# Kernel tuning notes

Measured on AMD Instinct MI355X. Metric: run time of the kernel, lower is better.

Reference implementation:

```python
import jax, jax.numpy as jnp
import numpy as np
import math

HEADS = 4
DK = 64            # dim // heads
TEMP = 1.0
LMAX = 2048        # max segment length (for padded ragged attention)


def setup_inputs() -> dict:
    key = jax.random.key(0)
    ks = jax.random.split(key, 6)
    T, H, B = 1024, 256, 16
    # ragged lengths alternating 2048/1024 -> N = 24576
    lengths = np.tile(np.array([2048, 1024], dtype=np.int64), B // 2)
    N = int(lengths.sum())
    s = 1.0 / math.sqrt(H)
    return {
        "go_mat": jax.random.normal(ks[0], (T, H), jnp.float32),
        "node_h": jax.random.normal(ks[1], (N, H), jnp.float32),
        "Wq": jax.random.normal(ks[2], (H, H), jnp.float32) * s,
        "Wk": jax.random.normal(ks[3], (H, H), jnp.float32) * s,
        "Wv": jax.random.normal(ks[4], (H, H), jnp.float32) * s,
        "Wproj": jax.random.normal(ks[5], (H, H), jnp.float32) * s,
        "num_nodes_per_graph": jnp.asarray(lengths),
    }


def reference(go_mat, node_h, Wq, Wk, Wv, Wproj, num_nodes_per_graph):
    lengths = num_nodes_per_graph
    B = lengths.shape[0]
    N, H = node_h.shape
    T = go_mat.shape[0]

    # segment bookkeeping: graph id and within-graph offset for each node
    cum = jnp.cumsum(lengths)                       # [B]
    starts = cum - lengths                          # [B]
    g = jnp.searchsorted(cum, jnp.arange(N), side="right")  # [N] graph id
    off = jnp.arange(N) - starts[g]                 # [N] position within graph

    # projections (torch Linear: x @ W.T)
    Q = (go_mat @ Wq.T).reshape(T, HEADS, DK).transpose(1, 0, 2)   # [h,T,dk]
    K = node_h @ Wk.T                                              # [N,H]
    V = node_h @ Wv.T

    # scatter packed nodes into padded [B, Lmax, H]
    Kp = jnp.zeros((B, LMAX, H), K.dtype).at[g, off].set(K)
    Vp = jnp.zeros((B, LMAX, H), V.dtype).at[g, off].set(V)
    Kp = Kp.reshape(B, LMAX, HEADS, DK).transpose(0, 2, 1, 3)      # [B,h,L,dk]
    Vp = Vp.reshape(B, LMAX, HEADS, DK).transpose(0, 2, 1, 3)

    scores = jnp.einsum("htd,bhld->bhtl", Q, Kp) / (math.sqrt(DK) * TEMP)
    valid = jnp.arange(LMAX)[None, :] < lengths[:, None]           # [B,L]
    scores = jnp.where(valid[:, None, None, :], scores, jnp.float32(-1e30))
    attn = jax.nn.softmax(scores, axis=-1)                         # [B,h,T,L]

    ctx = jnp.einsum("bhtl,bhld->bhtd", attn, Vp)                  # [B,h,T,dk]
    ctx = ctx.transpose(0, 2, 1, 3).reshape(B, T, H)               # [B,T,H]
    return ctx @ Wproj.T
```

## Files before the change

### kernel.cpp

```cpp
#include <hip/hip_runtime.h>
#include <math.h>

#define HEADS 4
#define DK 64
#define HD 256

typedef __attribute__((ext_vector_type(8))) __bf16 bf16x8;
typedef __attribute__((ext_vector_type(4))) float floatx4;

__device__ __forceinline__ ushort f2bf(float f) {
  union { float f; unsigned u; } x; x.f = f;
  return (ushort)((x.u + 0x7FFF + ((x.u >> 16) & 1)) >> 16);
}

#if __has_builtin(__builtin_amdgcn_exp2f)
#define EXP2(x) __builtin_amdgcn_exp2f(x)
#else
#define EXP2(x) exp2f(x)
#endif

__device__ __forceinline__ unsigned pack_bf2(float lo, float hi) {
  union { float f; unsigned u; } a, b;
  a.f = lo; b.f = hi;
  return __builtin_amdgcn_perm(b.u + 0x8000u, a.u + 0x8000u, 0x07060302u);
}

#define GLDS(g, l) __builtin_amdgcn_global_load_lds(                      \
    (const __attribute__((address_space(1))) unsigned*)(g),               \
    (__attribute__((address_space(3))) unsigned*)(l), 16, 0, 0)

__global__ __launch_bounds__(256) void cvt_all(const float* __restrict__ go,
                                               const float* __restrict__ nh,
                                               ushort* __restrict__ gobf,
                                               ushort* __restrict__ nodebf,
                                               int T, int N) {
  const int idx = blockIdx.x * 256 + threadIdx.x;
  const int row = idx >> 5, gr = idx & 31;
  if (row >= T + N) return;
  const float* x; ushort* y; int r;
  if (row < T) { x = go; y = gobf; r = row; }
  else         { x = nh; y = nodebf; r = row - T; }
  const int chunk = gr >> 3, g = gr & 7;
  const float* src = x + (size_t)r * 256 + gr * 8;
  float4 a = *(const float4*)src;
  float4 bq = *(const float4*)(src + 4);
  const int phys = g ^ (r & 7);
  ushort* dst = y + (size_t)r * 256 + chunk * 64 + phys * 8;
  ushort4 o0 = {f2bf(a.x), f2bf(a.y), f2bf(a.z), f2bf(a.w)};
  ushort4 o1 = {f2bf(bq.x), f2bf(bq.y), f2bf(bq.z), f2bf(bq.w)};
  *(ushort4*)dst = o0;
  *(ushort4*)(dst + 4) = o1;
}

__global__ __launch_bounds__(256) void cvt_swz_w(const float* __restrict__ w0,
                                                 const float* __restrict__ w1,
                                                 const float* __restrict__ w2,
                                                 const float* __restrict__ w3,
                                                 ushort* __restrict__ y) {
  const float* srcs[4] = {w0, w1, w2, w3};
  const float* x = srcs[blockIdx.y];
  ushort* yo = y + (size_t)blockIdx.y * HD * HD;
  const int idx = blockIdx.x * 256 + threadIdx.x;
  const int row = idx >> 5, gr = idx & 31;
  const int chunk = gr >> 3, g = gr & 7;
  const float* src = x + (size_t)row * 256 + gr * 8;
  float4 a = *(const float4*)src;
  float4 bq = *(const float4*)(src + 4);
  const int phys = g ^ (row & 7);
  ushort* dst = yo + (size_t)row * 256 + chunk * 64 + phys * 8;
  ushort4 o0 = {f2bf(a.x), f2bf(a.y), f2bf(a.z), f2bf(a.w)};
  ushort4 o1 = {f2bf(bq.x), f2bf(bq.y), f2bf(bq.z), f2bf(bq.w)};
  *(ushort4*)dst = o0;
  *(ushort4*)(dst + 4) = o1;
}

template <int MODE>
__global__ __launch_bounds__(256) void gemm_bf16(const ushort* __restrict__ A,
                                                 const ushort* __restrict__ W,
                                                 ushort* __restrict__ C, int M,
                                                 int ldc) {
  __shared__ __align__(16) ushort As[128 * 64];
  __shared__ __align__(16) ushort Ws[64 * 64];
  const int tid = threadIdx.x, lane = tid & 63, w = tid >> 6;
  const int quad = lane >> 4, l15 = lane & 15;
  const int m0 = blockIdx.x * 128, n0 = blockIdx.y * 64;
  const int wm = w & 1, wn = w >> 1;

  floatx4 acc[4][2];
#pragma unroll
  for (int mt = 0; mt < 4; ++mt)
#pragma unroll
    for (int nt = 0; nt < 2; ++nt) acc[mt][nt] = (floatx4){0.f, 0.f, 0.f, 0.f};

  for (int k0 = 0; k0 < 256; k0 += 64) {
    __syncthreads();
#pragma unroll
    for (int t = 0; t < 4; ++t)
      GLDS(A + (size_t)(m0 + w * 32 + t * 8 + (lane >> 3)) * 256 + k0 + (lane & 7) * 8,
           &As[(w * 32 + t * 8) * 64]);
#pragma unroll
    for (int t = 0; t < 2; ++t)
      GLDS(W + (size_t)(n0 + w * 16 + t * 8 + (lane >> 3)) * 256 + k0 + (lane & 7) * 8,
           &Ws[(w * 16 + t * 8) * 64]);
    __syncthreads();

    bf16x8 af[4][2], bfr[2][2];
#pragma unroll
    for (int kk = 0; kk < 2; ++kk) {
      const int pg = ((kk * 4 + quad) ^ (l15 & 7)) * 8;
#pragma unroll
      for (int mt = 0; mt < 4; ++mt)
        af[mt][kk] = *(const bf16x8*)&As[(wm * 64 + mt * 16 + l15) * 64 + pg];
#pragma unroll
      for (int nt = 0; nt < 2; ++nt)
        bfr[nt][kk] = *(const bf16x8*)&Ws[(wn * 32 + nt * 16 + l15) * 64 + pg];
    }
#pragma unroll
    for (int kk = 0; kk < 2; ++kk)
#pragma unroll
      for (int mt = 0; mt < 4; ++mt)
#pragma unroll
        for (int nt = 0; nt < 2; ++nt)
          acc[mt][nt] = __builtin_amdgcn_mfma_f32_16x16x32_bf16(
              af[mt][kk], bfr[nt][kk], acc[mt][nt], 0, 0, 0);
  }

#pragma unroll
  for (int mt = 0; mt < 4; ++mt)
#pragma unroll
    for (int nt = 0; nt < 2; ++nt) {
      const int col = n0 + wn * 32 + nt * 16 + l15;
      if (MODE == 2) {
        const int d = col & 63;
        const int g = mt * 2 + (quad >> 1);
        const int node = m0 + wm * 64 + (g ^ (d & 7)) * 8 + (quad & 1) * 4;
        ushort4 o = {f2bf(acc[mt][nt][0]), f2bf(acc[mt][nt][1]),
                     f2bf(acc[mt][nt][2]), f2bf(acc[mt][nt][3])};
        *(ushort4*)&C[(size_t)col * ldc + node] = o;
      } else {
#pragma unroll
        for (int r = 0; r < 4; ++r) {
          const int row = m0 + wm * 64 + mt * 16 + quad * 4 + r;
          if (MODE == 3) {
            ((float*)C)[(size_t)row * 256 + col] = acc[mt][nt][r];
          } else {
            int cc = col;
            if (MODE == 1)
              cc = (col & ~63) | (((((col >> 3) & 7) ^ (row & 7))) << 3) | (col & 7);
            C[(size_t)row * 256 + cc] = f2bf(acc[mt][nt][r]);
          }
        }
      }
    }
}

__global__ __launch_bounds__(256, 3) void attn_split(
    const ushort* __restrict__ Qb, const ushort* __restrict__ Kg,
    const ushort* __restrict__ Vt, const int* __restrict__ lens,
    float* __restrict__ Opart, float* __restrict__ Lpart,
    int T, int N, int Bc) {
  __shared__ __align__(16) ushort Ks[2][64 * 64];
  __shared__ __align__(16) ushort Vs[2][64 * 64];
  __shared__ __align__(16) ushort Ps[4 * 32 * 72];

  const int tid = threadIdx.x, lane = tid & 63, wave = tid >> 6;
  const int quad = lane >> 4, l15 = lane & 15;
  const int h = blockIdx.y;

  int z = blockIdx.z, b, start = 0, len = 0, off = -1;
  for (b = 0; b < Bc; ++b) {
    len = lens[b];
    const int s = (len + 1023) >> 10;
    if (z < s) { off = z << 10; break; }
    z -= s; start += len;
  }
  if (off < 0) return;
  const int kcnt = min(1024, len - off);
  const int kbeg = start + off;

  const int q0 = blockIdx.x * 128 + wave * 32;
  bf16x8 qb[2][2];
#pragma unroll
  for (int qt = 0; qt < 2; ++qt)
#pragma unroll
    for (int kk = 0; kk < 2; ++kk)
      qb[qt][kk] = *(const bf16x8*)(Qb + (size_t)(q0 + qt * 16 + l15) * 256 +
                                    h * 64 + kk * 32 + quad * 8);

  floatx4 o[2][4];
#pragma unroll
  for (int qt = 0; qt < 2; ++qt)
#pragma unroll
    for (int nt = 0; nt < 4; ++nt) o[qt][nt] = (floatx4){0.f, 0.f, 0.f, 0.f};
  float lsum[2] = {0.f, 0.f};

  const float sc = 0.18033688011112042f;
  ushort* pw = &Ps[wave * 32 * 72];

  const int srow = lane >> 3;
  const int scol = (lane & 7) * 8;

  GLDS(Kg + (size_t)(kbeg + wave * 8 + srow) * 256 + h * 64 + scol,
       &Ks[0][(wave * 8) * 64]);
  GLDS(Kg + (size_t)(kbeg + wave * 8 + 32 + srow) * 256 + h * 64 + scol,
       &Ks[0][(wave * 8 + 32) * 64]);
  GLDS(Vt + (size_t)(h * 64 + wave * 8 + srow) * (size_t)N + kbeg + scol,
       &Vs[0][(wave * 8) * 64]);
  GLDS(Vt + (size_t)(h * 64 + wave * 8 + 32 + srow) * (size_t)N + kbeg + scol,
       &Vs[0][(wave * 8 + 32) * 64]);

  int buf = 0;
  for (int j0 = 0; j0 < kcnt; j0 += 64, buf ^= 1) {
    __syncthreads();
    const int jn = j0 + 64;
    if (jn < kcnt) {
      GLDS(Kg + (size_t)(kbeg + jn + wave * 8 + srow) * 256 + h * 64 + scol,
           &Ks[buf ^ 1][(wave * 8) * 64]);
      GLDS(Kg + (size_t)(kbeg + jn + wave * 8 + 32 + srow) * 256 + h * 64 + scol,
           &Ks[buf ^ 1][(wave * 8 + 32) * 64]);
      GLDS(Vt + (size_t)(h * 64 + wave * 8 + srow) * (size_t)N + kbeg + jn + scol,
           &Vs[buf ^ 1][(wave * 8) * 64]);
      GLDS(Vt + (size_t)(h * 64 + wave * 8 + 32 + srow) * (size_t)N + kbeg + jn + scol,
           &Vs[buf ^ 1][(wave * 8 + 32) * 64]);
    }

    floatx4 st[4][2];
#pragma unroll
    for (int t = 0; t < 4; ++t)
#pragma unroll
      for (int qt = 0; qt < 2; ++qt) st[t][qt] = (floatx4){0.f, 0.f, 0.f, 0.f};
#pragma unroll
    for (int kk = 0; kk < 2; ++kk) {
#pragma unroll
      for (int t = 0; t < 4; ++t) {
        bf16x8 kf = *(const bf16x8*)&Ks[buf][(t * 16 + l15) * 64 +
                                            ((kk * 4 + quad) ^ (l15 & 7)) * 8];
        st[t][0] = __builtin_amdgcn_mfma_f32_16x16x32_bf16(kf, qb[0][kk], st[t][0], 0, 0, 0);
        st[t][1] = __builtin_amdgcn_mfma_f32_16x16x32_bf16(kf, qb[1][kk], st[t][1], 0, 0, 0);
      }
    }

    if (jn <= kcnt) {
#pragma unroll
      for (int t = 0; t < 4; ++t)
#pragma unroll
        for (int qt = 0; qt < 2; ++qt) {
          float p[4];
#pragma unroll
          for (int r = 0; r < 4; ++r) p[r] = EXP2(fmaf(st[t][qt][r], sc, -32.0f));
          lsum[qt] += (p[0] + p[1]) + (p[2] + p[3]);
          uint2 pk = {pack_bf2(p[0], p[1]), pack_bf2(p[2], p[3])};
          *(uint2*)&pw[(qt * 16 + l15) * 72 + t * 16 + quad * 4] = pk;
        }
    } else {
#pragma unroll
      for (int t = 0; t < 4; ++t)
#pragma unroll
        for (int qt = 0; qt < 2; ++qt) {
          float p[4];
#pragma unroll
          for (int r = 0; r < 4; ++r) {
            const bool v = (j0 + t * 16 + quad * 4 + r) < kcnt;
            p[r] = v ? EXP2(fmaf(st[t][qt][r], sc, -32.0f)) : 0.0f;
          }
          lsum[qt] += (p[0] + p[1]) + (p[2] + p[3]);
          uint2 pk = {pack_bf2(p[0], p[1]), pack_bf2(p[2], p[3])};
          *(uint2*)&pw[(qt * 16 + l15) * 72 + t * 16 + quad * 4] = pk;
        }
    }

#pragma unroll
    for (int ks = 0; ks < 2; ++ks) {
      bf16x8 pa0 = *(const bf16x8*)&pw[l15 * 72 + ks * 32 + quad * 8];
      bf16x8 pa1 = *(const bf16x8*)&pw[(16 + l15) * 72 + ks * 32 + quad * 8];
#pragma unroll
      for (int nt = 0; nt < 4; ++nt) {
        bf16x8 vf = *(const bf16x8*)&Vs[buf][(nt * 16 + l15) * 64 +
                                            ((ks * 4 + quad) ^ (l15 & 7)) * 8];
        o[0][nt] = __builtin_amdgcn_mfma_f32_16x16x32_bf16(pa0, vf, o[0][nt], 0, 0, 0);
        o[1][nt] = __builtin_amdgcn_mfma_f32_16x16x32_bf16(pa1, vf, o[1][nt], 0, 0, 0);
      }
    }
  }

  const int part = (blockIdx.z * HEADS + h) * (T >> 7) + blockIdx.x;
  float* op = Opart + (size_t)part * (128 * 64);
#pragma unroll
  for (int qt = 0; qt < 2; ++qt) {
#pragma unroll
    for (int nt = 0; nt < 4; ++nt)
#pragma unroll
      for (int r = 0; r < 4; ++r)
        op[(wave * 32 + qt * 16 + quad * 4 + r) * 64 + nt * 16 + l15] = o[qt][nt][r];
    float lt = lsum[qt];
    lt += __shfl_xor(lt, 16);
    lt += __shfl_xor(lt, 32);
    if (lane < 16)
      Lpart[(size_t)part * 128 + wave * 32 + qt * 16 + lane] = lt;
  }
}

__global__ __launch_bounds__(256) void combine(const float* __restrict__ Opart,
                                               const float* __restrict__ Lpart,
                                               const int* __restrict__ lens,
                                               ushort* __restrict__ ctxb, int T) {
  const int t = threadIdx.x;
  const int row = blockIdx.x * 64 + (t >> 2);
  const int h = t & 3;
  const int b = row / T;
  const int tq = row - b * T;
  const int qx = tq >> 7, qr = tq & 127;
  const int QX = T >> 7;
  int z0 = 0;
  for (int i = 0; i < b; ++i) z0 += (lens[i] + 1023) >> 10;
  const int ns = (lens[b] + 1023) >> 10;

  float l = 0.f;
  float4 acc[16];
#pragma unroll
  for (int g = 0; g < 16; ++g) acc[g] = make_float4(0.f, 0.f, 0.f, 0.f);
  for (int s = 0; s < ns; ++s) {
    const size_t part = (size_t)((z0 + s) * HEADS + h) * QX + qx;
    l += Lpart[part * 128 + qr];
    const float4* src = (const float4*)(Opart + part * 8192 + (size_t)qr * 64);
#pragma unroll
    for (int g = 0; g < 16; ++g) {
      float4 v = src[g];
      acc[g].x += v.x; acc[g].y += v.y; acc[g].z += v.z; acc[g].w += v.w;
    }
  }
  const float inv = 1.0f / l;
  ushort* dst = ctxb + (size_t)row * 256 + h * 64;
#pragma unroll
  for (int gg = 0; gg < 8; ++gg) {
    const float4 a = acc[gg * 2], c = acc[gg * 2 + 1];
    const int phys = gg ^ (row & 7);
    ushort4 o0 = {f2bf(a.x * inv), f2bf(a.y * inv), f2bf(a.z * inv), f2bf(a.w * inv)};
    ushort4 o1 = {f2bf(c.x * inv), f2bf(c.y * inv), f2bf(c.z * inv), f2bf(c.w * inv)};
    *(ushort4*)&dst[phys * 8] = o0;
    *(ushort4*)&dst[phys * 8 + 4] = o1;
  }
}

extern "C" void kernel_launch(void* const* d_in, const int* in_sizes, int n_in,
                              void* d_out, int out_size, void* d_ws, size_t ws_size,
                              hipStream_t stream) {
  const float* go     = (const float*)d_in[0];
  const float* node_h = (const float*)d_in[1];
  const float* Wq     = (const float*)d_in[2];
  const float* Wk     = (const float*)d_in[3];
  const float* Wv     = (const float*)d_in[4];
  const float* Wproj  = (const float*)d_in[5];
  const int*   lens   = (const int*)d_in[6];

  const int T = in_sizes[0] / HD;
  const int N = in_sizes[1] / HD;
  const int B = in_sizes[6];
  const int NSPL = N >> 10;
  const int QX = T / 128;

  char* p = (char*)d_ws;
  ushort* Kgb  = (ushort*)p;  p += (size_t)N * HD * 2;
  ushort* Vtb  = (ushort*)p;  p += (size_t)N * HD * 2;
  ushort* Qbf  = (ushort*)p;  p += (size_t)T * HD * 2;
  ushort* gobf = (ushort*)p;  p += (size_t)T * HD * 2;
  ushort* ctxb = (ushort*)p;  p += (size_t)B * T * HD * 2;
  ushort* wbf  = (ushort*)p;  p += (size_t)4 * HD * HD * 2;
  ushort* wqbf = wbf;
  ushort* wkbf = wbf + (size_t)HD * HD;
  ushort* wvbf = wbf + (size_t)2 * HD * HD;
  ushort* wpbf = wbf + (size_t)3 * HD * HD;
  ushort* nodebf = (ushort*)p;
  float* Opart = (float*)p;   p += (size_t)NSPL * HEADS * QX * 8192 * 4;
  float* Lpart = (float*)p;   p += (size_t)NSPL * HEADS * QX * 128 * 4;

  cvt_all<<<((T + N) * 32 + 255) / 256, 256, 0, stream>>>(go, node_h, gobf, nodebf, T, N);
  cvt_swz_w<<<dim3(32, 4), 256, 0, stream>>>(Wq, Wk, Wv, Wproj, wbf);

  gemm_bf16<0><<<dim3(T / 128, 4), 256, 0, stream>>>(gobf, wqbf, Qbf, T, 0);
  gemm_bf16<1><<<dim3(N / 128, 4), 256, 0, stream>>>(nodebf, wkbf, Kgb, N, 0);
  gemm_bf16<2><<<dim3(N / 128, 4), 256, 0, stream>>>(nodebf, wvbf, Vtb, N, N);

  attn_split<<<dim3(QX, HEADS, NSPL), 256, 0, stream>>>(Qbf, Kgb, Vtb, lens,
                                                        Opart, Lpart, T, N, B);
  combine<<<(B * T) / 64, 256, 0, stream>>>(Opart, Lpart, lens, ctxb, T);

  gemm_bf16<3><<<dim3((B * T) / 128, 4), 256, 0, stream>>>(ctxb, wpbf, (ushort*)d_out, B * T, 0);
}
```

Measured before the change: 167.0 us.

## Fuse conversion and QKV launches, halve attention split size, store bf16 partials

Merges the input and weight conversion kernels into one launch and the three QKV projection GEMMs into a single launch. The attention key splits shrink from 1024 to 512 for more blocks, and K/V double buffering is dropped to raise occupancy (launch bound 5). The P tile in LDS becomes XOR-swizzled instead of padded. Partial outputs are stored as bf16 instead of fp32, and the combine kernel uses twice as many threads. This cuts launch overhead and partial-output traffic, but loses load/compute overlap in attention and adds bf16 rounding to the partials.

```diff
diff --git a/kernel.cpp b/kernel.cpp
--- a/kernel.cpp
+++ b/kernel.cpp
@@ -29,63 +29,42 @@
     (const __attribute__((address_space(1))) unsigned*)(g),               \
     (__attribute__((address_space(3))) unsigned*)(l), 16, 0, 0)
 
-__global__ __launch_bounds__(256) void cvt_all(const float* __restrict__ go,
-                                               const float* __restrict__ nh,
-                                               ushort* __restrict__ gobf,
-                                               ushort* __restrict__ nodebf,
-                                               int T, int N) {
+__global__ __launch_bounds__(256) void cvt_fused(
+    const float* __restrict__ go, const float* __restrict__ nh,
+    const float* __restrict__ w0, const float* __restrict__ w1,
+    const float* __restrict__ w2, const float* __restrict__ w3,
+    ushort* __restrict__ gobf, ushort* __restrict__ nodebf,
+    ushort* __restrict__ wbf, int T, int N) {
   const int idx = blockIdx.x * 256 + threadIdx.x;
   const int row = idx >> 5, gr = idx & 31;
-  if (row >= T + N) return;
-  const float* x; ushort* y; int r;
-  if (row < T) { x = go; y = gobf; r = row; }
-  else         { x = nh; y = nodebf; r = row - T; }
+  if (row >= T + N + 4 * 256) return;
+  const float* x; ushort* y; int r = row;
+  if (row < T) { x = go; y = gobf; }
+  else if (row < T + N) { x = nh; y = nodebf; r = row - T; }
+  else {
+    const int wr = row - T - N, wi = wr >> 8;
+    r = wr & 255;
+    x = (wi == 0) ? w0 : (wi == 1) ? w1 : (wi == 2) ? w2 : w3;
+    y = wbf + (size_t)wi * HD * HD;
+  }
   const int chunk = gr >> 3, g = gr & 7;
   const float* src = x + (size_t)r * 256 + gr * 8;
   float4 a = *(const float4*)src;
   float4 bq = *(const float4*)(src + 4);
-  const int phys = g ^ (r & 7);
-  ushort* dst = y + (size_t)r * 256 + chunk * 64 + phys * 8;
+  ushort* dst = y + (size_t)r * 256 + chunk * 64 + (g ^ (r & 7)) * 8;
   ushort4 o0 = {f2bf(a.x), f2bf(a.y), f2bf(a.z), f2bf(a.w)};
   ushort4 o1 = {f2bf(bq.x), f2bf(bq.y), f2bf(bq.z), f2bf(bq.w)};
   *(ushort4*)dst = o0;
   *(ushort4*)(dst + 4) = o1;
 }
 
-__global__ __launch_bounds__(256) void cvt_swz_w(const float* __restrict__ w0,
-                                                 const float* __restrict__ w1,
-                                                 const float* __restrict__ w2,
-                                                 const float* __restrict__ w3,
-                                                 ushort* __restrict__ y) {
-  const float* srcs[4] = {w0, w1, w2, w3};
-  const float* x = srcs[blockIdx.y];
-  ushort* yo = y + (size_t)blockIdx.y * HD * HD;
-  const int idx = blockIdx.x * 256 + threadIdx.x;
-  const int row = idx >> 5, gr = idx & 31;
-  const int chunk = gr >> 3, g = gr & 7;
-  const float* src = x + (size_t)row * 256 + gr * 8;
-  float4 a = *(const float4*)src;
-  float4 bq = *(const float4*)(src + 4);
-  const int phys = g ^ (row & 7);
-  ushort* dst = yo + (size_t)row * 256 + chunk * 64 + phys * 8;
-  ushort4 o0 = {f2bf(a.x), f2bf(a.y), f2bf(a.z), f2bf(a.w)};
-  ushort4 o1 = {f2bf(bq.x), f2bf(bq.y), f2bf(bq.z), f2bf(bq.w)};
-  *(ushort4*)dst = o0;
-  *(ushort4*)(dst + 4) = o1;
-}
-
-template <int MODE>
-__global__ __launch_bounds__(256) void gemm_bf16(const ushort* __restrict__ A,
-                                                 const ushort* __restrict__ W,
-                                                 ushort* __restrict__ C, int M,
-                                                 int ldc) {
-  __shared__ __align__(16) ushort As[128 * 64];
-  __shared__ __align__(16) ushort Ws[64 * 64];
-  const int tid = threadIdx.x, lane = tid & 63, w = tid >> 6;
-  const int quad = lane >> 4, l15 = lane & 15;
-  const int m0 = blockIdx.x * 128, n0 = blockIdx.y * 64;
+__device__ __forceinline__ void gemm_tile(const ushort* __restrict__ A,
+                                          const ushort* __restrict__ W,
+                                          ushort* __restrict__ C, int m0,
+                                          int n0, int mode, int ldc,
+                                          ushort* As, ushort* Ws, int lane,
+                                          int w, int quad, int l15) {
   const int wm = w & 1, wn = w >> 1;
-
   floatx4 acc[4][2];
 #pragma unroll
   for (int mt = 0; mt < 4; ++mt)
@@ -130,7 +109,7 @@
 #pragma unroll
     for (int nt = 0; nt < 2; ++nt) {
       const int col = n0 + wn * 32 + nt * 16 + l15;
-      if (MODE == 2) {
+      if (mode == 2) {
         const int d = col & 63;
         const int g = mt * 2 + (quad >> 1);
         const int node = m0 + wm * 64 + (g ^ (d & 7)) * 8 + (quad & 1) * 4;
@@ -141,11 +120,11 @@
 #pragma unroll
         for (int r = 0; r < 4; ++r) {
           const int row = m0 + wm * 64 + mt * 16 + quad * 4 + r;
-          if (MODE == 3) {
+          if (mode == 3) {
             ((float*)C)[(size_t)row * 256 + col] = acc[mt][nt][r];
           } else {
             int cc = col;
-            if (MODE == 1)
+            if (mode == 1)
               cc = (col & ~63) | (((((col >> 3) & 7) ^ (row & 7))) << 3) | (col & 7);
             C[(size_t)row * 256 + cc] = f2bf(acc[mt][nt][r]);
           }
@@ -154,28 +133,52 @@
     }
 }
 
-__global__ __launch_bounds__(256, 3) void attn_split(
+__global__ __launch_bounds__(256) void qkv_gemm(const ushort* __restrict__ gobf,
+                                                const ushort* __restrict__ nodebf,
+                                                const ushort* __restrict__ wbf,
+                                                ushort* __restrict__ Qbf,
+                                                ushort* __restrict__ Kgb,
+                                                ushort* __restrict__ Vtb,
+                                                int T, int N) {
+  __shared__ __align__(16) ushort As[128 * 64];
+  __shared__ __align__(16) ushort Ws[64 * 64];
+  const int tid = threadIdx.x, lane = tid & 63, w = tid >> 6;
+  const int quad = lane >> 4, l15 = lane & 15;
+  const int QX = T >> 7, KB = N >> 7;
+  const int jx = blockIdx.x >> 2, n0 = (blockIdx.x & 3) * 64;
+  if (jx < QX)
+    gemm_tile(gobf, wbf, Qbf, jx * 128, n0, 0, 0, As, Ws, lane, w, quad, l15);
+  else if (jx < QX + KB)
+    gemm_tile(nodebf, wbf + (size_t)HD * HD, Kgb, (jx - QX) * 128, n0, 1, 0,
+              As, Ws, lane, w, quad, l15);
+  else
+    gemm_tile(nodebf, wbf + (size_t)2 * HD * HD, Vtb, (jx - QX - KB) * 128, n0,
+              2, N, As, Ws, lane, w, quad, l15);
+}
+
+__global__ __launch_bounds__(256, 5) void attn_split(
     const ushort* __restrict__ Qb, const ushort* __restrict__ Kg,
     const ushort* __restrict__ Vt, const int* __restrict__ lens,
-    float* __restrict__ Opart, float* __restrict__ Lpart,
-    int T, int N, int Bc) {
-  __shared__ __align__(16) ushort Ks[2][64 * 64];
-  __shared__ __align__(16) ushort Vs[2][64 * 64];
-  __shared__ __align__(16) ushort Ps[4 * 32 * 72];
+    ushort* __restrict__ Opart, float* __restrict__ Lpart,
+    int T, int N, int B) {
+  __shared__ __align__(16) ushort Ks[64 * 64];
+  __shared__ __align__(16) ushort Vs[64 * 64];
+  __shared__ __align__(16) ushort Ps[4 * 32 * 64];
 
   const int tid = threadIdx.x, lane = tid & 63, wave = tid >> 6;
   const int quad = lane >> 4, l15 = lane & 15;
   const int h = blockIdx.y;
+  const int QX = T >> 7;
 
   int z = blockIdx.z, b, start = 0, len = 0, off = -1;
-  for (b = 0; b < Bc; ++b) {
+  for (b = 0; b < B; ++b) {
     len = lens[b];
-    const int s = (len + 1023) >> 10;
-    if (z < s) { off = z << 10; break; }
+    const int s = (len + 511) >> 9;
+    if (z < s) { off = z << 9; break; }
     z -= s; start += len;
   }
   if (off < 0) return;
-  const int kcnt = min(1024, len - off);
+  const int kcnt = min(512, len - off);
   const int kbeg = start + off;
 
   const int q0 = blockIdx.x * 128 + wave * 32;
@@ -195,34 +198,21 @@
   float lsum[2] = {0.f, 0.f};
 
   const float sc = 0.18033688011112042f;
-  ushort* pw = &Ps[wave * 32 * 72];
-
+  ushort* pw = &Ps[wave * 32 * 64];
   const int srow = lane >> 3;
   const int scol = (lane & 7) * 8;
 
-  GLDS(Kg + (size_t)(kbeg + wave * 8 + srow) * 256 + h * 64 + scol,
-       &Ks[0][(wave * 8) * 64]);
-  GLDS(Kg + (size_t)(kbeg + wave * 8 + 32 + srow) * 256 + h * 64 + scol,
-       &Ks[0][(wave * 8 + 32) * 64]);
-  GLDS(Vt + (size_t)(h * 64 + wave * 8 + srow) * (size_t)N + kbeg + scol,
-       &Vs[0][(wave * 8) * 64]);
-  GLDS(Vt + (size_t)(h * 64 + wave * 8 + 32 + srow) * (size_t)N + kbeg + scol,
-       &Vs[0][(wave * 8 + 32) * 64]);
-
-  int buf = 0;
-  for (int j0 = 0; j0 < kcnt; j0 += 64, buf ^= 1) {
+  for (int j0 = 0; j0 < kcnt; j0 += 64) {
     __syncthreads();
-    const int jn = j0 + 64;
-    if (jn < kcnt) {
-      GLDS(Kg + (size_t)(kbeg + jn + wave * 8 + srow) * 256 + h * 64 + scol,
-           &Ks[buf ^ 1][(wave * 8) * 64]);
-      GLDS(Kg + (size_t)(kbeg + jn + wave * 8 + 32 + srow) * 256 + h * 64 + scol,
-           &Ks[buf ^ 1][(wave * 8 + 32) * 64]);
-      GLDS(Vt + (size_t)(h * 64 + wave * 8 + srow) * (size_t)N + kbeg + jn + scol,
-           &Vs[buf ^ 1][(wave * 8) * 64]);
-      GLDS(Vt + (size_t)(h * 64 + wave * 8 + 32 + srow) * (size_t)N + kbeg + jn + scol,
-           &Vs[buf ^ 1][(wave * 8 + 32) * 64]);
-    }
+    GLDS(Kg + (size_t)(kbeg + j0 + wave * 8 + srow) * 256 + h * 64 + scol,
+         &Ks[(wave * 8) * 64]);
+    GLDS(Kg + (size_t)(kbeg + j0 + wave * 8 + 32 + srow) * 256 + h * 64 + scol,
+         &Ks[(wave * 8 + 32) * 64]);
+    GLDS(Vt + (size_t)(h * 64 + wave * 8 + srow) * (size_t)N + kbeg + j0 + scol,
+         &Vs[(wave * 8) * 64]);
+    GLDS(Vt + (size_t)(h * 64 + wave * 8 + 32 + srow) * (size_t)N + kbeg + j0 + scol,
+         &Vs[(wave * 8 + 32) * 64]);
+    __syncthreads();
 
     floatx4 st[4][2];
 #pragma unroll
@@ -233,13 +223,14 @@
     for (int kk = 0; kk < 2; ++kk) {
 #pragma unroll
       for (int t = 0; t < 4; ++t) {
-        bf16x8 kf = *(const bf16x8*)&Ks[buf][(t * 16 + l15) * 64 +
-                                            ((kk * 4 + quad) ^ (l15 & 7)) * 8];
+        bf16x8 kf = *(const bf16x8*)&Ks[(t * 16 + l15) * 64 +
+                                        ((kk * 4 + quad) ^ (l15 & 7)) * 8];
         st[t][0] = __builtin_amdgcn_mfma_f32_16x16x32_bf16(kf, qb[0][kk], st[t][0], 0, 0, 0);
         st[t][1] = __builtin_amdgcn_mfma_f32_16x16x32_bf16(kf, qb[1][kk], st[t][1], 0, 0, 0);
       }
     }
 
+    const int jn = j0 + 64;
     if (jn <= kcnt) {
 #pragma unroll
       for (int t = 0; t < 4; ++t)
@@ -250,7 +241,8 @@
           for (int r = 0; r < 4; ++r) p[r] = EXP2(fmaf(st[t][qt][r], sc, -32.0f));
           lsum[qt] += (p[0] + p[1]) + (p[2] + p[3]);
           uint2 pk = {pack_bf2(p[0], p[1]), pack_bf2(p[2], p[3])};
-          *(uint2*)&pw[(qt * 16 + l15) * 72 + t * 16 + quad * 4] = pk;
+          const int phys = (t * 2 + (quad >> 1)) ^ (l15 & 7);
+          *(uint2*)&pw[(qt * 16 + l15) * 64 + phys * 8 + (quad & 1) * 4] = pk;
         }
     } else {
 #pragma unroll
@@ -265,33 +257,35 @@
           }
           lsum[qt] += (p[0] + p[1]) + (p[2] + p[3]);
           uint2 pk = {pack_bf2(p[0], p[1]), pack_bf2(p[2], p[3])};
-          *(uint2*)&pw[(qt * 16 + l15) * 72 + t * 16 + quad * 4] = pk;
+          const int phys = (t * 2 + (quad >> 1)) ^ (l15 & 7);
+          *(uint2*)&pw[(qt * 16 + l15) * 64 + phys * 8 + (quad & 1) * 4] = pk;
         }
     }
 
 #pragma unroll
     for (int ks = 0; ks < 2; ++ks) {
-      bf16x8 pa0 = *(const bf16x8*)&pw[l15 * 72 + ks * 32 + quad * 8];
-      bf16x8 pa1 = *(const bf16x8*)&pw[(16 + l15) * 72 + ks * 32 + quad * 8];
+      bf16x8 pa0 = *(const bf16x8*)&pw[l15 * 64 + ((ks * 4 + quad) ^ (l15 & 7)) * 8];
+      bf16x8 pa1 = *(const bf16x8*)&pw[(16 + l15) * 64 + ((ks * 4 + quad) ^ (l15 & 7)) * 8];
 #pragma unroll
       for (int nt = 0; nt < 4; ++nt) {
-        bf16x8 vf = *(const bf16x8*)&Vs[buf][(nt * 16 + l15) * 64 +
-                                            ((ks * 4 + quad) ^ (l15 & 7)) * 8];
+        bf16x8 vf = *(const bf16x8*)&Vs[(nt * 16 + l15) * 64 +
+                                        ((ks * 4 + quad) ^ (l15 & 7)) * 8];
         o[0][nt] = __builtin_amdgcn_mfma_f32_16x16x32_bf16(pa0, vf, o[0][nt], 0, 0, 0);
         o[1][nt] = __builtin_amdgcn_mfma_f32_16x16x32_bf16(pa1, vf, o[1][nt], 0, 0, 0);
       }
     }
   }
 
-  const int part = (blockIdx.z * HEADS + h) * (T >> 7) + blockIdx.x;
-  float* op = Opart + (size_t)part * (128 * 64);
+  const int part = (blockIdx.z * HEADS + h) * QX + blockIdx.x;
+  ushort* op = Opart + (size_t)part * 8192;
 #pragma unroll
   for (int qt = 0; qt < 2; ++qt) {
 #pragma unroll
     for (int nt = 0; nt < 4; ++nt)
 #pragma unroll
       for (int r = 0; r < 4; ++r)
-        op[(wave * 32 + qt * 16 + quad * 4 + r) * 64 + nt * 16 + l15] = o[qt][nt][r];
+        op[(wave * 32 + qt * 16 + quad * 4 + r) * 64 + nt * 16 + l15] =
+            f2bf(o[qt][nt][r]);
     float lt = lsum[qt];
     lt += __shfl_xor(lt, 16);
     lt += __shfl_xor(lt, 32);
@@ -300,46 +294,70 @@
   }
 }
 
-__global__ __launch_bounds__(256) void combine(const float* __restrict__ Opart,
+__global__ __launch_bounds__(256) void combine(const ushort* __restrict__ Opart,
                                                const float* __restrict__ Lpart,
                                                const int* __restrict__ lens,
-                                               ushort* __restrict__ ctxb, int T) {
-  const int t = threadIdx.x;
-  const int row = blockIdx.x * 64 + (t >> 2);
-  const int h = t & 3;
+                                               ushort* __restrict__ ctxb, int T,
+                                               int B) {
+  const int item = blockIdx.x * 256 + threadIdx.x;
+  if (item >= B * T * 8) return;
+  const int half = item & 1;
+  const int h = (item >> 1) & 3;
+  const int row = item >> 3;
   const int b = row / T;
   const int tq = row - b * T;
   const int qx = tq >> 7, qr = tq & 127;
   const int QX = T >> 7;
   int z0 = 0;
-  for (int i = 0; i < b; ++i) z0 += (lens[i] + 1023) >> 10;
-  const int ns = (lens[b] + 1023) >> 10;
+  for (int i = 0; i < b; ++i) z0 += (lens[i] + 511) >> 9;
+  const int ns = (lens[b] + 511) >> 9;
 
   float l = 0.f;
-  float4 acc[16];
-#pragma unroll
-  for (int g = 0; g < 16; ++g) acc[g] = make_float4(0.f, 0.f, 0.f, 0.f);
+  float acc[32];
+#pragma unroll
+  for (int g = 0; g < 32; ++g) acc[g] = 0.f;
   for (int s = 0; s < ns; ++s) {
     const size_t part = (size_t)((z0 + s) * HEADS + h) * QX + qx;
     l += Lpart[part * 128 + qr];
-    const float4* src = (const float4*)(Opart + part * 8192 + (size_t)qr * 64);
-#pragma unroll
-    for (int g = 0; g < 16; ++g) {
-      float4 v = src[g];
-      acc[g].x += v.x; acc[g].y += v.y; acc[g].z += v.z; acc[g].w += v.w;
+    const uint4* src =
+        (const uint4*)(Opart + part * 8192 + (size_t)qr * 64 + half * 32);
+#pragma unroll
+    for (int k = 0; k < 4; ++k) {
+      uint4 raw = src[k];
+      const unsigned uu[4] = {raw.x, raw.y, raw.z, raw.w};
+#pragma unroll
+      for (int j = 0; j < 4; ++j) {
+        union { unsigned u; float f; } lo, hi;
+        lo.u = uu[j] << 16;
+        hi.u = uu[j] & 0xFFFF0000u;
+        acc[k * 8 + j * 2] += lo.f;
+        acc[k * 8 + j * 2 + 1] += hi.f;
+      }
     }
   }
   const float inv = 1.0f / l;
   ushort* dst = ctxb + (size_t)row * 256 + h * 64;
 #pragma unroll
-  for (int gg = 0; gg < 8; ++gg) {
-    const float4 a = acc[gg * 2], c = acc[gg * 2 + 1];
-    const int phys = gg ^ (row & 7);
-    ushort4 o0 = {f2bf(a.x * inv), f2bf(a.y * inv), f2bf(a.z * inv), f2bf(a.w * inv)};
-    ushort4 o1 = {f2bf(c.x * inv), f2bf(c.y * inv), f2bf(c.z * inv), f2bf(c.w * inv)};
+  for (int gg = 0; gg < 4; ++gg) {
+    const int phys = (half * 4 + gg) ^ (row & 7);
+    ushort4 o0 = {f2bf(acc[gg * 8 + 0] * inv), f2bf(acc[gg * 8 + 1] * inv),
+                  f2bf(acc[gg * 8 + 2] * inv), f2bf(acc[gg * 8 + 3] * inv)};
+    ushort4 o1 = {f2bf(acc[gg * 8 + 4] * inv), f2bf(acc[gg * 8 + 5] * inv),
+                  f2bf(acc[gg * 8 + 6] * inv), f2bf(acc[gg * 8 + 7] * inv)};
     *(ushort4*)&dst[phys * 8] = o0;
     *(ushort4*)&dst[phys * 8 + 4] = o1;
   }
+}
+
+__global__ __launch_bounds__(256) void proj_gemm(const ushort* __restrict__ ctxb,
+                                                 const ushort* __restrict__ wbf,
+                                                 float* __restrict__ outp) {
+  __shared__ __align__(16) ushort As[128 * 64];
+  __shared__ __align__(16) ushort Ws[64 * 64];
+  const int tid = threadIdx.x, lane = tid & 63, w = tid >> 6;
+  const int quad = lane >> 4, l15 = lane & 15;
+  gemm_tile(ctxb, wbf + (size_t)3 * HD * HD, (ushort*)outp, blockIdx.x * 128,
+            blockIdx.y * 64, 3, 0, As, Ws, lane, w, quad, l15);
 }
 
 extern "C" void kernel_launch(void* const* d_in, const int* in_sizes, int n_in,
@@ -356,8 +374,9 @@
   const int T = in_sizes[0] / HD;
   const int N = in_sizes[1] / HD;
   const int B = in_sizes[6];
-  const int NSPL = N >> 10;
-  const int QX = T / 128;
+  const int NSPL = N >> 9;
+  const int QX = T >> 7;
+  const int KB = N >> 7;
 
   char* p = (char*)d_ws;
   ushort* Kgb  = (ushort*)p;  p += (size_t)N * HD * 2;
@@ -366,24 +385,20 @@
   ushort* gobf = (ushort*)p;  p += (size_t)T * HD * 2;
   ushort* ctxb = (ushort*)p;  p += (size_t)B * T * HD * 2;
   ushort* wbf  = (ushort*)p;  p += (size_t)4 * HD * HD * 2;
-  ushort* wqbf = wbf;
-  ushort* wkbf = wbf + (size_t)HD * HD;
-  ushort* wvbf = wbf + (size_t)2 * HD * HD;
-  ushort* wpbf = wbf + (size_t)3 * HD * HD;
   ushort* nodebf = (ushort*)p;
-  float* Opart = (float*)p;   p += (size_t)NSPL * HEADS * QX * 8192 * 4;
+  ushort* Opart = (ushort*)p; p += (size_t)NSPL * HEADS * QX * 8192 * 2;
   float* Lpart = (float*)p;   p += (size_t)NSPL * HEADS * QX * 128 * 4;
 
-  cvt_all<<<((T + N) * 32 + 255) / 256, 256, 0, stream>>>(go, node_h, gobf, nodebf, T, N);
-  cvt_swz_w<<<dim3(32, 4), 256, 0, stream>>>(Wq, Wk, Wv, Wproj, wbf);
-
-  gemm_bf16<0><<<dim3(T / 128, 4), 256, 0, stream>>>(gobf, wqbf, Qbf, T, 0);
-  gemm_bf16<1><<<dim3(N / 128, 4), 256, 0, stream>>>(nodebf, wkbf, Kgb, N, 0);
-  gemm_bf16<2><<<dim3(N / 128, 4), 256, 0, stream>>>(nodebf, wvbf, Vtb, N, N);
+  cvt_fused<<<((T + N + 1024) * 32 + 255) / 256, 256, 0, stream>>>(
+      go, node_h, Wq, Wk, Wv, Wproj, gobf, nodebf, wbf, T, N);
+
+  qkv_gemm<<<(QX + 2 * KB) * 4, 256, 0, stream>>>(gobf, nodebf, wbf, Qbf, Kgb,
+                                                  Vtb, T, N);
 
   attn_split<<<dim3(QX, HEADS, NSPL), 256, 0, stream>>>(Qbf, Kgb, Vtb, lens,
                                                         Opart, Lpart, T, N, B);
-  combine<<<(B * T) / 64, 256, 0, stream>>>(Opart, Lpart, lens, ctxb, T);
-
-  gemm_bf16<3><<<dim3((B * T) / 128, 4), 256, 0, stream>>>(ctxb, wpbf, (ushort*)d_out, B * T, 0);
-}
+
+  combine<<<(B * T * 8) / 256, 256, 0, stream>>>(Opart, Lpart, lens, ctxb, T, B);
+
+  proj_gemm<<<dim3((B * T) / 128, 4), 256, 0, stream>>>(ctxb, wbf, (float*)d_out);
+}
```

Result: slower. 230.7 us (+38.1%).
